# Performance work log

Hardware: AMD Instinct MI355X
Metric: run time of the kernel (lower is better)

## Reference

```python
import jax, jax.numpy as jnp
import numpy as np

N, F_IN, HID, H1, E = 50000, 512, 128, 4, 800000
NEG_SLOPE = 0.2

def setup_inputs() -> dict:
    key = jax.random.key(0)
    ks = jax.random.split(key, 10)
    s = lambda fan: 1.0 / np.sqrt(fan)
    x = jax.random.normal(ks[0], (N, F_IN), jnp.float32)
    edge_index = jax.random.randint(ks[1], (2, E), 0, N, jnp.int32)
    W1 = jax.random.normal(ks[2], (F_IN, H1 * HID), jnp.float32) * s(F_IN)
    a_src1 = jax.random.normal(ks[3], (H1, HID), jnp.float32) * s(HID)
    a_dst1 = jax.random.normal(ks[4], (H1, HID), jnp.float32) * s(HID)
    b1 = jnp.zeros((H1 * HID,), jnp.float32)
    W2 = jax.random.normal(ks[5], (H1 * HID, HID), jnp.float32) * s(H1 * HID)
    a_src2 = jax.random.normal(ks[6], (1, HID), jnp.float32) * s(HID)
    a_dst2 = jax.random.normal(ks[7], (1, HID), jnp.float32) * s(HID)
    b2 = jnp.zeros((HID,), jnp.float32)
    return {"x": x, "edge_index": edge_index, "W1": W1, "a_src1": a_src1,
            "a_dst1": a_dst1, "b1": b1, "W2": W2, "a_src2": a_src2,
            "a_dst2": a_dst2, "b2": b2}

def _gat(x, src, dst, W, a_src, a_dst, b, n):
    H, C = a_src.shape
    h = (x @ W).reshape(-1, H, C)                      # [N, H, C]
    # per-edge attention logits: alpha_src[src] + alpha_dst[dst]
    e = jax.nn.leaky_relu((h * a_src).sum(-1)[src] + (h * a_dst).sum(-1)[dst],
                          NEG_SLOPE)                   # [E', H]
    # segment softmax over destination node
    m = jax.ops.segment_max(e, dst, num_segments=n)
    p = jnp.exp(e - m[dst])
    denom = jax.ops.segment_sum(p, dst, num_segments=n)
    alpha = p / (denom[dst] + 1e-16)
    # weighted scatter-add aggregation
    out = jax.ops.segment_sum(h[src] * alpha[:, :, None], dst, num_segments=n)
    return out.reshape(-1, H * C) + b

def reference(x, edge_index, W1, a_src1, a_dst1, b1, W2, a_src2, a_dst2, b2):
    loops = jnp.arange(N, dtype=edge_index.dtype)      # add_self_loops=True
    src = jnp.concatenate([edge_index[0], loops])
    dst = jnp.concatenate([edge_index[1], loops])
    h = jax.nn.elu(_gat(x, src, dst, W1, a_src1, a_dst1, b1, N))
    return _gat(h, src, dst, W2, a_src2, a_dst2, b2, N)
```

## Files before the change

kernel.cpp:

```cpp
#include <hip/hip_runtime.h>
#include <hip/hip_bf16.h>
#include <math.h>

#define NEG_SLOPE 0.2f

constexpr int N_NODES = 50000;
constexpr int F_IN    = 512;
constexpr int HID     = 128;
constexpr int H1      = 4;
constexpr int E_EDGES = 800000;
constexpr int E_TOT   = E_EDGES + N_NODES;
constexpr int DEG_CAP = 64;

typedef __attribute__((ext_vector_type(8))) short short8;
typedef __attribute__((ext_vector_type(4))) float floatx4;
typedef __attribute__((ext_vector_type(2))) float f32x2;
typedef __attribute__((ext_vector_type(4))) unsigned short ushort4v;
typedef __attribute__((ext_vector_type(8))) unsigned short ushort8v;

__device__ __forceinline__ unsigned short f2bf(float f) {
  union { float f; unsigned int u; } v; v.f = f;
  unsigned int u = v.u + 0x7FFFu + ((v.u >> 16) & 1u);
  return (unsigned short)(u >> 16);
}
__device__ __forceinline__ float bf_lo(unsigned int u) {
  union { unsigned int u; float f; } v; v.u = u << 16; return v.f;
}
__device__ __forceinline__ float bf_hi(unsigned int u) {
  union { unsigned int u; float f; } v; v.u = u & 0xFFFF0000u; return v.f;
}

template <int CPT>
__device__ __forceinline__ void store_vec(unsigned short* p, const float* v) {
#pragma unroll
  for (int c = 0; c < CPT; c += 4) {
    ushort4v o;
#pragma unroll
    for (int j = 0; j < 4; ++j) o[j] = f2bf(v[c + j]);
    *(ushort4v*)(p + c) = o;
  }
}
template <int CPT>
__device__ __forceinline__ void store_vec(float* p, const float* v) {
#pragma unroll
  for (int c = 0; c < CPT; c += 4) *(float4*)(p + c) = *(const float4*)(v + c);
}

__device__ __forceinline__ void async_load16(const void* g, void* lds) {
  __builtin_amdgcn_global_load_lds(
      (const __attribute__((address_space(1))) unsigned int*)g,
      (__attribute__((address_space(3))) unsigned int*)lds, 16, 0, 0);
}

__global__ void prep_kernel(const float* __restrict__ W1, const float* __restrict__ W2,
                            unsigned short* __restrict__ W1t, unsigned short* __restrict__ W2t,
                            int* __restrict__ cnt) {
  int i = blockIdx.x * 256 + threadIdx.x;
  if (i < N_NODES) cnt[i] = 0;
  int j = i - N_NODES;
  if (j >= 0 && j < 512 * 512) {
    int n = j >> 9, k = j & 511;
    W1t[j] = f2bf(W1[k * 512 + n]);
  }
  int l = i - N_NODES - 512 * 512;
  if (l >= 0 && l < 128 * 512) {
    int n = l >> 9, k = l & 511;
    W2t[l] = f2bf(W2[k * 128 + n]);
  }
}

template <bool CVT_A, bool FILL, int BM>
__global__ __launch_bounds__(256) void gemm_bf16_kernel(
    const void* __restrict__ Araw, const unsigned short* __restrict__ Bt,
    unsigned short* __restrict__ C, const float* __restrict__ a_srcp,
    const float* __restrict__ a_dstp,
    float* __restrict__ alpha_src, float* __restrict__ alpha_dst,
    int M, int N, int K, int Hn, int nRowTiles,
    const int* __restrict__ ei, int* __restrict__ cnt, int* __restrict__ adj,
    int gemmBlocks) {
  constexpr int NWAVES = BM / 32;
  constexpr int WMW    = BM / 64;
  constexpr int BPW    = 8 / NWAVES;
  __shared__ __align__(16) unsigned char smem[BM * 132 * 2];
  unsigned short* As = (unsigned short*)smem;
  unsigned short* Bs = (unsigned short*)(smem + BM * 64);
  unsigned short* Cs = (unsigned short*)smem;
  __shared__ float red_s[128][2];
  __shared__ float red_d[128][2];

  if (FILL && blockIdx.x >= gemmBlocks) {
    int i = (blockIdx.x - gemmBlocks) * 256 + threadIdx.x;
    if (i < E_TOT) {
      int s, d;
      if (i < E_EDGES) { s = ei[i]; d = ei[E_EDGES + i]; }
      else             { s = i - E_EDGES; d = s; }
      int pos = atomicAdd(&cnt[d], 1);
      if (pos < DEG_CAP) adj[d * DEG_CAP + pos] = s;
    }
    return;
  }

  int grp = blockIdx.x / (8 * Hn);
  int w8 = blockIdx.x % (8 * Hn);
  int head = w8 >> 3;
  int rowTile = grp * 8 + (w8 & 7);
  if (rowTile >= nRowTiles) return;
  int row0 = rowTile * BM;
  int col0 = head * 128;

  int tid = threadIdx.x;
  int lane = tid & 63, wave = tid >> 6;
  int wm = wave % WMW, wn = wave / WMW;
  int l15 = lane & 15, quad = lane >> 4;

  floatx4 acc[4][4];
#pragma unroll
  for (int i = 0; i < 4; ++i)
#pragma unroll
    for (int j = 0; j < 4; ++j) acc[i][j] = (floatx4){0.f, 0.f, 0.f, 0.f};

  int r_in = (lane >> 2);
  int c8sw = (((lane & 3) ^ ((lane >> 3) & 3)) * 8);
  int sqrd = (quad ^ ((l15 >> 1) & 3)) * 8;

  for (int k0 = 0; k0 < K; k0 += 32) {
#pragma unroll
    for (int p = 0; p < BPW; ++p) {
      int seg = wave * BPW + p;
      int r = seg * 16 + r_in;
      int gc = col0 + r;
      async_load16(Bt + (size_t)gc * K + k0 + c8sw, &Bs[seg * 512]);
    }
    if constexpr (CVT_A) {
      const float* Af = (const float*)Araw;
#pragma unroll
      for (int p = 0; p < 4; ++p) {
        int lin = tid + p * 256;
        int r = lin >> 3;
        int q = lin & 7;
        int gr = row0 + r; if (gr >= M) gr = M - 1;
        float4 f = *(const float4*)(Af + (size_t)gr * K + k0 + q * 4);
        ushort4v o;
        o[0] = f2bf(f.x); o[1] = f2bf(f.y); o[2] = f2bf(f.z); o[3] = f2bf(f.w);
        int sl = ((q >> 1) ^ ((lin >> 4) & 3));
        *(ushort4v*)&As[r * 32 + sl * 8 + (q & 1) * 4] = o;
      }
    } else {
      const unsigned short* Ab = (const unsigned short*)Araw;
#pragma unroll
      for (int p = 0; p < 2; ++p) {
        int seg = wave * 2 + p;
        int r = seg * 16 + r_in;
        int gr = row0 + r; if (gr >= M) gr = M - 1;
        async_load16(Ab + (size_t)gr * K + k0 + c8sw, &As[seg * 512]);
      }
    }
    __syncthreads();

    short8 a[4], b[4];
#pragma unroll
    for (int mi = 0; mi < 4; ++mi)
      a[mi] = *(const short8*)&As[(wm * 64 + mi * 16 + l15) * 32 + sqrd];
#pragma unroll
    for (int ni = 0; ni < 4; ++ni)
      b[ni] = *(const short8*)&Bs[(wn * 64 + ni * 16 + l15) * 32 + sqrd];
#pragma unroll
    for (int mi = 0; mi < 4; ++mi)
#pragma unroll
      for (int ni = 0; ni < 4; ++ni)
        acc[mi][ni] = __builtin_amdgcn_mfma_f32_16x16x32_bf16(a[mi], b[ni], acc[mi][ni], 0, 0, 0);
    __syncthreads();
  }

  float a_s[4], a_d[4];
#pragma unroll
  for (int ni = 0; ni < 4; ++ni) {
    int cih = wn * 64 + ni * 16 + l15;
    a_s[ni] = a_srcp[head * HID + cih];
    a_d[ni] = a_dstp[head * HID + cih];
  }

#pragma unroll
  for (int mi = 0; mi < 4; ++mi) {
#pragma unroll
    for (int r = 0; r < 4; ++r) {
      int rloc = wm * 64 + mi * 16 + quad * 4 + r;
      float ps = 0.f, pd = 0.f;
#pragma unroll
      for (int ni = 0; ni < 4; ++ni) {
        float v = acc[mi][ni][r];
        ps += v * a_s[ni];
        pd += v * a_d[ni];
        Cs[rloc * 132 + wn * 64 + ni * 16 + l15] = f2bf(v);
      }
#pragma unroll
      for (int off = 1; off < 16; off <<= 1) {
        ps += __shfl_xor(ps, off);
        pd += __shfl_xor(pd, off);
      }
      if (l15 == 0) { red_s[rloc][wn] = ps; red_d[rloc][wn] = pd; }
    }
  }
  __syncthreads();

  {
    int row = tid >> 1;
    int cc  = (tid & 1) * 64;
    int grow = row0 + row;
    if (grow < M) {
      const unsigned short* src = &Cs[row * 132 + cc];
      unsigned short* dst = &C[(size_t)grow * N + col0 + cc];
#pragma unroll
      for (int c = 0; c < 64; c += 8)
        *(ushort8v*)(dst + c) = *(const ushort8v*)(src + c);
    }
  }
  if (tid < BM) {
    int grow = row0 + tid;
    if (grow < M) {
      alpha_src[(size_t)grow * Hn + head] = red_s[tid][0] + red_s[tid][1];
      alpha_dst[(size_t)grow * Hn + head] = red_d[tid][0] + red_d[tid][1];
    }
  }
}

template <int H, typename OT>
__global__ __launch_bounds__(64) void aggregate_kernel(
    const unsigned short* __restrict__ h, const float* __restrict__ asrc,
    const float* __restrict__ adst, const int* __restrict__ cnt,
    const int* __restrict__ adj, const float* __restrict__ bias,
    OT* __restrict__ out, int apply_elu) {
  constexpr int CPT = 8;
  constexpr int CH = H * HID;
  constexpr int NCH = CH / CPT;
  constexpr int SLOTS = 64 / NCH;
  __shared__ float p_sh[64 * H];
  __shared__ int ro_sh[64];

  const int node = blockIdx.x;
  const int lane = threadIdx.x;
  int deg = cnt[node];
  if (deg > DEG_CAP) deg = DEG_CAP;

  int s_i = 0;
  if (lane < deg) s_i = adj[node * DEG_CAP + lane];
  ro_sh[lane] = s_i * (CH * 2);
  float ar[H];
  if constexpr (H == 4) {
    float4 f = (lane < deg) ? *(const float4*)(asrc + (size_t)s_i * 4)
                            : make_float4(0.f, 0.f, 0.f, 0.f);
    ar[0] = f.x; ar[1] = f.y; ar[2] = f.z; ar[3] = f.w;
  } else {
    ar[0] = (lane < deg) ? asrc[s_i] : 0.f;
  }
  asm volatile("s_waitcnt lgkmcnt(0)" ::: "memory");

  const int chlane = lane % NCH;
  const int slot = lane / NCH;
  const int ch = chlane * CPT;
  const int head = ch >> 7;
  const char* hb = (const char*)h + ch * 2;

  auto loadu = [&](uint4& U, int e) {
    if (e < deg) U = *(const uint4*)(hb + (unsigned)ro_sh[e]);
    else         U = make_uint4(0u, 0u, 0u, 0u);
  };

  uint4 u0, u1, u2, u3, u4, u5, u6, u7;
  loadu(u0, slot);             loadu(u1, slot + SLOTS);
  loadu(u2, slot + 2 * SLOTS); loadu(u3, slot + 3 * SLOTS);
  loadu(u4, slot + 4 * SLOTS); loadu(u5, slot + 5 * SLOTS);
  loadu(u6, slot + 6 * SLOTS); loadu(u7, slot + 7 * SLOTS);

#pragma unroll
  for (int hh = 0; hh < H; ++hh) {
    float v = ar[hh] + adst[node * H + hh];
    v = (v > 0.f) ? v : NEG_SLOPE * v;
    float lg = (lane < deg) ? v : -1e30f;
#pragma unroll
    for (int o = 32; o; o >>= 1) lg = fmaxf(lg, __shfl_xor(lg, o));
    float p = (lane < deg) ? __expf(v - lg) : 0.f;
    float s = p;
#pragma unroll
    for (int o = 32; o; o >>= 1) s += __shfl_xor(s, o);
    p_sh[lane * H + hh] = p * (1.f / (s + 1e-16f));
  }
  asm volatile("s_waitcnt lgkmcnt(0)" ::: "memory");

  f32x2 ac0 = {0.f, 0.f}, ac1 = {0.f, 0.f}, ac2v = {0.f, 0.f}, ac3 = {0.f, 0.f};
  auto consume = [&](const uint4& U, int e) {
    float w = p_sh[(e & 63) * H + head];
    f32x2 wp = {w, w};
    f32x2 t;
    t.x = bf_lo(U.x); t.y = bf_hi(U.x); ac0  += t * wp;
    t.x = bf_lo(U.y); t.y = bf_hi(U.y); ac1  += t * wp;
    t.x = bf_lo(U.z); t.y = bf_hi(U.z); ac2v += t * wp;
    t.x = bf_lo(U.w); t.y = bf_hi(U.w); ac3  += t * wp;
  };

  int base = 0;
  for (;;) {
    int nb = base + 8 * SLOTS;
    if (nb < deg) {
      consume(u0, base + slot);             loadu(u0, nb + slot);
      consume(u1, base + slot + SLOTS);     loadu(u1, nb + slot + SLOTS);
      consume(u2, base + slot + 2 * SLOTS); loadu(u2, nb + slot + 2 * SLOTS);
      consume(u3, base + slot + 3 * SLOTS); loadu(u3, nb + slot + 3 * SLOTS);
      consume(u4, base + slot + 4 * SLOTS); loadu(u4, nb + slot + 4 * SLOTS);
      consume(u5, base + slot + 5 * SLOTS); loadu(u5, nb + slot + 5 * SLOTS);
      consume(u6, base + slot + 6 * SLOTS); loadu(u6, nb + slot + 6 * SLOTS);
      consume(u7, base + slot + 7 * SLOTS); loadu(u7, nb + slot + 7 * SLOTS);
      base = nb;
    } else {
      consume(u0, base + slot);             consume(u1, base + slot + SLOTS);
      consume(u2, base + slot + 2 * SLOTS); consume(u3, base + slot + 3 * SLOTS);
      consume(u4, base + slot + 4 * SLOTS); consume(u5, base + slot + 5 * SLOTS);
      consume(u6, base + slot + 6 * SLOTS); consume(u7, base + slot + 7 * SLOTS);
      break;
    }
  }

#pragma unroll
  for (int o = NCH; o < 64; o <<= 1) {
    ac0.x  += __shfl_xor(ac0.x, o);  ac0.y  += __shfl_xor(ac0.y, o);
    ac1.x  += __shfl_xor(ac1.x, o);  ac1.y  += __shfl_xor(ac1.y, o);
    ac2v.x += __shfl_xor(ac2v.x, o); ac2v.y += __shfl_xor(ac2v.y, o);
    ac3.x  += __shfl_xor(ac3.x, o);  ac3.y  += __shfl_xor(ac3.y, o);
  }

  if (slot == 0) {
    float r[CPT] = {ac0.x, ac0.y, ac1.x, ac1.y, ac2v.x, ac2v.y, ac3.x, ac3.y};
#pragma unroll
    for (int c = 0; c < CPT; ++c) {
      float t = r[c] + bias[ch + c];
      if (apply_elu) t = (t > 0.f) ? t : (__expf(t) - 1.f);
      r[c] = t;
    }
    store_vec<CPT>(&out[(size_t)node * CH + ch], r);
  }
}

extern "C" void kernel_launch(void* const* d_in, const int* in_sizes, int n_in,
                              void* d_out, int out_size, void* d_ws, size_t ws_size,
                              hipStream_t stream) {
  const float* x      = (const float*)d_in[0];
  const int*   ei     = (const int*)d_in[1];
  const float* W1     = (const float*)d_in[2];
  const float* a_src1 = (const float*)d_in[3];
  const float* a_dst1 = (const float*)d_in[4];
  const float* b1     = (const float*)d_in[5];
  const float* W2     = (const float*)d_in[6];
  const float* a_src2 = (const float*)d_in[7];
  const float* a_dst2 = (const float*)d_in[8];
  const float* b2     = (const float*)d_in[9];
  float* out = (float*)d_out;

  float* ws   = (float*)d_ws;
  float* as1  = ws;
  float* ad1  = as1 + N_NODES * H1;
  float* as2  = ad1 + N_NODES * H1;
  float* ad2  = as2 + N_NODES;
  unsigned short* bufA = (unsigned short*)(ad2 + N_NODES);
  unsigned short* bufB = bufA + (size_t)N_NODES * 512;
  unsigned short* hmidb = bufA;
  unsigned short* h1b   = bufB;
  unsigned short* h2b   = bufB;
  unsigned short* W1t   = bufB + (size_t)N_NODES * 512;
  unsigned short* W2t   = W1t + 512 * 512;
  int* cnt = (int*)(W2t + 128 * 512);
  int* adj = cnt + N_NODES;

  constexpr int NRT = (N_NODES + 127) / 128;
  constexpr int NRT8 = ((NRT + 7) / 8) * 8;
  constexpr int NRT2 = (N_NODES + 63) / 64;
  constexpr int NRT2_8 = ((NRT2 + 7) / 8) * 8;
  constexpr int PREP_ITEMS = N_NODES + 512 * 512 + 128 * 512;
  constexpr int FILL_BLOCKS = (E_TOT + 255) / 256;
  constexpr int GEMM1_BLOCKS = NRT8 * H1;

  prep_kernel<<<(PREP_ITEMS + 255) / 256, 256, 0, stream>>>(W1, W2, W1t, W2t, cnt);

  gemm_bf16_kernel<true, true, 128>
      <<<GEMM1_BLOCKS + FILL_BLOCKS, 256, 0, stream>>>(
      x, W1t, h1b, a_src1, a_dst1, as1, ad1, N_NODES, 512, 512, H1, NRT,
      ei, cnt, adj, GEMM1_BLOCKS);
  aggregate_kernel<4, unsigned short><<<N_NODES, 64, 0, stream>>>(
      h1b, as1, ad1, cnt, adj, b1, hmidb, 1);

  gemm_bf16_kernel<false, false, 64><<<NRT2_8, 128, 0, stream>>>(
      hmidb, W2t, h2b, a_src2, a_dst2, as2, ad2, N_NODES, 128, 512, 1, NRT2,
      nullptr, nullptr, nullptr, 0);
  aggregate_kernel<1, float><<<N_NODES, 64, 0, stream>>>(
      h2b, as2, ad2, cnt, adj, b2, out, 0);
}
```

Baseline: 464.4 us.

## Use dedicated 128x256 tile GEMM1 kernel covering two heads per block

Adds a specialized layer-1 GEMM kernel where each block computes a 128x256 output tile (two attention heads) instead of 128x128. Each converted fp32 A tile is reused across twice as many columns, which halves the redundant fp32 reads and bf16 conversions of x. It also fuses the per-head alpha_src/alpha_dst dot products and the edge-list fill blocks into the same launch. The cost is more accumulator registers per thread (4x8 MFMA tiles) and more LDS, which may lower occupancy.

```diff
diff --git a/kernel.cpp b/kernel.cpp
--- a/kernel.cpp
+++ b/kernel.cpp
@@ -66,6 +66,148 @@
   if (l >= 0 && l < 128 * 512) {
     int n = l >> 9, k = l & 511;
     W2t[l] = f2bf(W2[k * 128 + n]);
+  }
+}
+
+template <bool FILL>
+__global__ __launch_bounds__(256) void gemm1_2h_kernel(
+    const float* __restrict__ A, const unsigned short* __restrict__ Bt,
+    unsigned short* __restrict__ C, const float* __restrict__ a_srcp,
+    const float* __restrict__ a_dstp,
+    float* __restrict__ alpha_src, float* __restrict__ alpha_dst,
+    int M, int nRowTiles,
+    const int* __restrict__ ei, int* __restrict__ cnt, int* __restrict__ adj,
+    int gemmBlocks) {
+  constexpr int K = 512, N = 512;
+  __shared__ __align__(16) unsigned char smem[128 * 260 * 2];
+  unsigned short* As = (unsigned short*)smem;
+  unsigned short* Bs = (unsigned short*)(smem + 8192);
+  unsigned short* Cs = (unsigned short*)smem;
+  __shared__ float red_s[128][2];
+  __shared__ float red_d[128][2];
+
+  if (FILL && blockIdx.x >= gemmBlocks) {
+    int i = (blockIdx.x - gemmBlocks) * 256 + threadIdx.x;
+    if (i < E_TOT) {
+      int s, d;
+      if (i < E_EDGES) { s = ei[i]; d = ei[E_EDGES + i]; }
+      else             { s = i - E_EDGES; d = s; }
+      int pos = atomicAdd(&cnt[d], 1);
+      if (pos < DEG_CAP) adj[d * DEG_CAP + pos] = s;
+    }
+    return;
+  }
+
+  int grp = blockIdx.x / 16;
+  int w8 = blockIdx.x % 16;
+  int hp = w8 >> 3;
+  int rowTile = grp * 8 + (w8 & 7);
+  if (rowTile >= nRowTiles) return;
+  int row0 = rowTile * 128;
+  int col0 = hp * 256;
+
+  int tid = threadIdx.x;
+  int lane = tid & 63, wave = tid >> 6;
+  int wm = wave & 1, wn = wave >> 1;
+  int l15 = lane & 15, quad = lane >> 4;
+
+  floatx4 acc[4][8];
+#pragma unroll
+  for (int i = 0; i < 4; ++i)
+#pragma unroll
+    for (int j = 0; j < 8; ++j) acc[i][j] = (floatx4){0.f, 0.f, 0.f, 0.f};
+
+  int r_in = (lane >> 2);
+  int c8sw = (((lane & 3) ^ ((lane >> 3) & 3)) * 8);
+  int sqrd = (quad ^ ((l15 >> 1) & 3)) * 8;
+
+  for (int k0 = 0; k0 < K; k0 += 32) {
+#pragma unroll
+    for (int p = 0; p < 4; ++p) {
+      int seg = wave * 4 + p;
+      int r = seg * 16 + r_in;
+      int gc = col0 + r;
+      async_load16(Bt + (size_t)gc * K + k0 + c8sw, &Bs[seg * 512]);
+    }
+#pragma unroll
+    for (int p = 0; p < 4; ++p) {
+      int lin = tid + p * 256;
+      int r = lin >> 3;
+      int q = lin & 7;
+      int gr = row0 + r; if (gr >= M) gr = M - 1;
+      float4 f = *(const float4*)(A + (size_t)gr * K + k0 + q * 4);
+      ushort4v o;
+      o[0] = f2bf(f.x); o[1] = f2bf(f.y); o[2] = f2bf(f.z); o[3] = f2bf(f.w);
+      int sl = ((q >> 1) ^ ((lin >> 4) & 3));
+      *(ushort4v*)&As[r * 32 + sl * 8 + (q & 1) * 4] = o;
+    }
+    __syncthreads();
+
+    short8 a[4], b[8];
+#pragma unroll
+    for (int mi = 0; mi < 4; ++mi)
+      a[mi] = *(const short8*)&As[(wm * 64 + mi * 16 + l15) * 32 + sqrd];
+#pragma unroll
+    for (int ni = 0; ni < 8; ++ni)
+      b[ni] = *(const short8*)&Bs[(wn * 128 + ni * 16 + l15) * 32 + sqrd];
+#pragma unroll
+    for (int mi = 0; mi < 4; ++mi)
+#pragma unroll
+      for (int ni = 0; ni < 8; ++ni)
+        acc[mi][ni] = __builtin_amdgcn_mfma_f32_16x16x32_bf16(a[mi], b[ni], acc[mi][ni], 0, 0, 0);
+    __syncthreads();
+  }
+
+  float a_s[8], a_d[8];
+#pragma unroll
+  for (int ni = 0; ni < 8; ++ni) {
+    int cih = ni * 16 + l15;
+    a_s[ni] = a_srcp[(hp * 2 + wn) * HID + cih];
+    a_d[ni] = a_dstp[(hp * 2 + wn) * HID + cih];
+  }
+
+#pragma unroll
+  for (int mi = 0; mi < 4; ++mi) {
+#pragma unroll
+    for (int r = 0; r < 4; ++r) {
+      int rloc = wm * 64 + mi * 16 + quad * 4 + r;
+      float ps = 0.f, pd = 0.f;
+#pragma unroll
+      for (int ni = 0; ni < 8; ++ni) {
+        float v = acc[mi][ni][r];
+        ps += v * a_s[ni];
+        pd += v * a_d[ni];
+        Cs[rloc * 260 + wn * 128 + ni * 16 + l15] = f2bf(v);
+      }
+#pragma unroll
+      for (int off = 1; off < 16; off <<= 1) {
+        ps += __shfl_xor(ps, off);
+        pd += __shfl_xor(pd, off);
+      }
+      if (l15 == 0) { red_s[rloc][wn] = ps; red_d[rloc][wn] = pd; }
+    }
+  }
+  __syncthreads();
+
+  {
+    int row = tid >> 1;
+    int cc  = (tid & 1) * 128;
+    int grow = row0 + row;
+    if (grow < M) {
+      const unsigned short* src = &Cs[row * 260 + cc];
+      unsigned short* dst = &C[(size_t)grow * N + col0 + cc];
+#pragma unroll
+      for (int c = 0; c < 128; c += 8)
+        *(ushort8v*)(dst + c) = *(const ushort8v*)(src + c);
+    }
+  }
+  {
+    int rrow = tid & 127, h = tid >> 7;
+    int grow = row0 + rrow;
+    if (grow < M) {
+      alpha_src[(size_t)grow * H1 + hp * 2 + h] = red_s[rrow][h];
+      alpha_dst[(size_t)grow * H1 + hp * 2 + h] = red_d[rrow][h];
+    }
   }
 }
 
@@ -131,21 +273,7 @@
       int gc = col0 + r;
       async_load16(Bt + (size_t)gc * K + k0 + c8sw, &Bs[seg * 512]);
     }
-    if constexpr (CVT_A) {
-      const float* Af = (const float*)Araw;
-#pragma unroll
-      for (int p = 0; p < 4; ++p) {
-        int lin = tid + p * 256;
-        int r = lin >> 3;
-        int q = lin & 7;
-        int gr = row0 + r; if (gr >= M) gr = M - 1;
-        float4 f = *(const float4*)(Af + (size_t)gr * K + k0 + q * 4);
-        ushort4v o;
-        o[0] = f2bf(f.x); o[1] = f2bf(f.y); o[2] = f2bf(f.z); o[3] = f2bf(f.w);
-        int sl = ((q >> 1) ^ ((lin >> 4) & 3));
-        *(ushort4v*)&As[r * 32 + sl * 8 + (q & 1) * 4] = o;
-      }
-    } else {
+    {
       const unsigned short* Ab = (const unsigned short*)Araw;
 #pragma unroll
       for (int p = 0; p < 2; ++p) {
@@ -376,13 +504,12 @@
   constexpr int NRT2_8 = ((NRT2 + 7) / 8) * 8;
   constexpr int PREP_ITEMS = N_NODES + 512 * 512 + 128 * 512;
   constexpr int FILL_BLOCKS = (E_TOT + 255) / 256;
-  constexpr int GEMM1_BLOCKS = NRT8 * H1;
+  constexpr int GEMM1_BLOCKS = NRT8 * 2;
 
   prep_kernel<<<(PREP_ITEMS + 255) / 256, 256, 0, stream>>>(W1, W2, W1t, W2t, cnt);
 
-  gemm_bf16_kernel<true, true, 128>
-      <<<GEMM1_BLOCKS + FILL_BLOCKS, 256, 0, stream>>>(
-      x, W1t, h1b, a_src1, a_dst1, as1, ad1, N_NODES, 512, 512, H1, NRT,
+  gemm1_2h_kernel<true><<<GEMM1_BLOCKS + FILL_BLOCKS, 256, 0, stream>>>(
+      x, W1t, h1b, a_src1, a_dst1, as1, ad1, N_NODES, NRT,
       ei, cnt, adj, GEMM1_BLOCKS);
   aggregate_kernel<4, unsigned short><<<N_NODES, 64, 0, stream>>>(
       h1b, as1, ad1, cnt, adj, b1, hmidb, 1);
```

Measured after the change: 516.0 us. 11.1% more time.
